# Optimization experiments

Hardware: AMD Instinct MI355X
Metric: run time of the kernel (lower is better)

Reference implementation:

```python
import jax, jax.numpy as jnp
import numpy as np


def _ln(x, w, b, eps=1e-5):
    m = x.mean(-1, keepdims=True)
    v = jnp.mean((x - m) ** 2, axis=-1, keepdims=True)
    return (x - m) * jax.lax.rsqrt(v + eps) * w + b


def _to_seq(xc, g):
    # xc: [B,Di,H,W] -> [B,L,Di]; g0: row-major fwd, g1: row-major rev,
    # g2: col-major fwd, g3: col-major rev (CrossScan_1..4)
    if g >= 2:
        xc = xc.transpose(0, 1, 3, 2)
    s = xc.reshape(xc.shape[0], xc.shape[1], -1)
    if g % 2 == 1:
        s = jnp.flip(s, -1)
    return s.transpose(0, 2, 1)


def _from_seq(y, g, H, W):
    # y: [B,L,Di] -> [B,H,W,Di], inverse of _to_seq (CrossMerge_1..4)
    if g % 2 == 1:
        y = jnp.flip(y, 1)
    Bn, L, Di = y.shape
    if g >= 2:
        return y.reshape(Bn, W, H, Di).transpose(0, 2, 1, 3)
    return y.reshape(Bn, H, W, Di)


def _sscan(dA, dBx, Cm):
    # selective scan: h_t = dA_t*h + dBx_t ; y_t = <h_t, C_t>
    # dA,dBx: [B,L,Di,S], Cm: [B,L,S] -> y: [B,L,Di]
    def step(h, inp):
        a, bx, c = inp
        h = a * h + bx
        return h, jnp.einsum('bds,bs->bd', h, c)
    h0 = jnp.zeros(dA.shape[:1] + dA.shape[2:], dA.dtype)
    _, ys = jax.lax.scan(step, h0, (dA.transpose(1, 0, 2, 3), dBx.transpose(1, 0, 2, 3), Cm.transpose(1, 0, 2)))
    return ys.transpose(1, 0, 2)


def _ss2d(xc, g, H, W, ipw, ipb, cw, cb, xpw, dtw, dtb, A_log, Ds, onw, onb, opw, opb):
    R = dtw.shape[-1]
    S = A_log.shape[-1]
    xz = xc @ ipw.T + ipb                      # [B,H,W,2*Di]
    Di = xz.shape[-1] // 2
    xi, z = xz[..., :Di], xz[..., Di:]
    xi = xi.transpose(0, 3, 1, 2)              # [B,Di,H,W]
    xi = jax.lax.conv_general_dilated(xi, cw, (1, 1), [(1, 1), (1, 1)],
                                      dimension_numbers=('NCHW', 'OIHW', 'NCHW'),
                                      feature_group_count=Di) + cb[None, :, None, None]
    xi = jax.nn.silu(xi)
    seq = _to_seq(xi, g)                       # [B,L,Di]
    xdbl = seq @ xpw.T                         # [B,L,R+2S]
    dtr, Bm, Cm = xdbl[..., :R], xdbl[..., R:R + S], xdbl[..., R + S:]
    dt = jax.nn.softplus(dtr @ dtw.T + dtb)    # [B,L,Di]
    A = -jnp.exp(A_log)                        # [Di,S]
    dA = jnp.exp(dt[..., None] * A)            # [B,L,Di,S]
    dBx = (dt * seq)[..., None] * Bm[:, :, None, :]
    y = _sscan(dA, dBx, Cm) + Ds * seq
    y = _from_seq(y, g, H, W)                  # [B,H,W,Di]
    y = _ln(y, onw, onb)
    y = y * jax.nn.silu(z)
    return y @ opw.T + opb


def setup_inputs() -> dict:
    Bn, Hh, Ww, C = 8, 96, 96, 256
    Di = C // 4
    S = 1
    R = max(1, (Di + 15) // 16)
    key = jax.random.key(0)
    ks = jax.random.split(key, 12)
    nrm = lambda k, sh, s: jax.random.normal(k, sh, jnp.float32) * s
    return {
        'x': nrm(ks[0], (Bn, Hh * Ww, C), 1.0),
        'norm_w': jnp.ones((C,), jnp.float32), 'norm_b': jnp.zeros((C,), jnp.float32),
        'fc_w': nrm(ks[1], (C, C), 0.02), 'fc_b': jnp.zeros((C,), jnp.float32),
        'conv1d_w': nrm(ks[2], (1, 1, 3), 0.3),
        'in_proj_w': nrm(ks[3], (4, 2 * Di, Di), 0.05), 'in_proj_b': jnp.zeros((4, 2 * Di), jnp.float32),
        'conv2d_w': nrm(ks[4], (4, Di, 1, 3, 3), 0.2), 'conv2d_b': jnp.zeros((4, Di), jnp.float32),
        'x_proj_w': nrm(ks[5], (4, R + 2 * S, Di), 0.05),
        'dt_w': nrm(ks[6], (4, Di, R), 0.1), 'dt_b': nrm(ks[7], (4, Di), 0.1),
        'A_log': nrm(ks[8], (4, Di, S), 0.1),
        'Ds': jnp.ones((4, Di), jnp.float32),
        'out_norm_w': jnp.ones((4, Di), jnp.float32), 'out_norm_b': jnp.zeros((4, Di), jnp.float32),
        'out_proj_w': nrm(ks[9], (4, Di, Di), 0.05), 'out_proj_b': jnp.zeros((4, Di), jnp.float32),
        'proj_w': nrm(ks[10], (C, C), 0.02), 'proj_b': jnp.zeros((C,), jnp.float32),
        'skip_scale': jnp.ones((1,), jnp.float32),
        'H': Hh, 'W': Ww,
    }


def reference(x, norm_w, norm_b, fc_w, fc_b, conv1d_w, in_proj_w, in_proj_b, conv2d_w, conv2d_b,
              x_proj_w, dt_w, dt_b, A_log, Ds, out_norm_w, out_norm_b, out_proj_w, out_proj_b,
              proj_w, proj_b, skip_scale, H, W):
    B, N, C = x.shape
    xn = _ln(x, norm_w, norm_b)
    z_avg = xn.mean(1)                         # [B,C] (permute(0,2,1).mean(2))
    yg = jax.lax.conv_general_dilated(z_avg[:, None, :], conv1d_w, (1,), [(1, 1)],
                                      dimension_numbers=('NCH', 'OIH', 'NCH'))[:, 0, :]
    gate = jax.nn.sigmoid(z_avg @ fc_w.T + fc_b + yg)   # fc_out_2 [B,C]
    xg = xn.reshape(B, H, W, C)
    Dg = C // 4
    outs = [_ss2d(xg[..., g * Dg:(g + 1) * Dg], g, H, W,
                  in_proj_w[g], in_proj_b[g], conv2d_w[g], conv2d_b[g], x_proj_w[g],
                  dt_w[g], dt_b[g], A_log[g], Ds[g], out_norm_w[g], out_norm_b[g],
                  out_proj_w[g], out_proj_b[g]) for g in range(4)]
    xm = jnp.concatenate(outs, -1) * skip_scale * xg
    xm = xm.reshape(B, N, C) * gate[:, None, :]
    xm = _ln(xm, norm_w, norm_b)
    return xm @ proj_w.T + proj_b
```

## Files before the change

### kernel.cpp

```cpp
#include <hip/hip_runtime.h>
#include <math.h>

#define HH 96
#define WWI 96
#define NN 9216
#define CC 256
#define LL 9216
#define CHK 96
#define NCH 96
#define BB 8
#define BN (BB*NN)

__device__ __forceinline__ float softplusf(float x){
    float e = expf(-fabsf(x));
    return fmaxf(x, 0.f) + log1pf(e);
}
__device__ __forceinline__ float sigmf(float x){ return 1.f / (1.f + expf(-x)); }

__device__ __forceinline__ float wredsum(float v){
    #pragma unroll
    for(int o = 32; o > 0; o >>= 1) v += __shfl_xor(v, o, 64);
    return v;
}

__device__ __forceinline__ void wredsum2(float& s, float& q){
    #pragma unroll
    for(int o = 32; o > 0; o >>= 1){
        s += __shfl_xor(s, o, 64);
        q += __shfl_xor(q, o, 64);
    }
}

__device__ __forceinline__ void chunk_walk(int g, int chunk, int& base, int& step){
    if(g == 0){ base = chunk * 96;        step = 1;   }
    else if(g == 1){ base = 9215 - chunk * 96; step = -1; }
    else if(g == 2){ base = chunk;        step = 96;  }
    else { base = 9215 - chunk;           step = -96; }
}

__global__ __launch_bounds__(256) void k_stats(const float* __restrict__ x,
                                               float* __restrict__ mrs){
    int wid = threadIdx.x >> 6, lane = threadIdx.x & 63;
    size_t row = (size_t)blockIdx.x * 4 + wid;
    float4 v = ((const float4*)(x + row * CC))[lane];
    float s = wredsum(v.x + v.y + v.z + v.w);
    float q = wredsum(v.x*v.x + v.y*v.y + v.z*v.z + v.w*v.w);
    float m = s * (1.f/256.f);
    float var = q * (1.f/256.f) - m*m;
    float rs = rsqrtf(fmaxf(var, 0.f) + 1e-5f);
    if(lane == 0){ mrs[2*row] = m; mrs[2*row+1] = rs; }
}

__global__ __launch_bounds__(256) void k_stats2(const float* __restrict__ y,
                                                float* __restrict__ mrs2){
    int wid = threadIdx.x >> 6, lane = threadIdx.x & 63;
    size_t row = (size_t)blockIdx.x * 4 + wid;
    size_t b = row / NN, n = row - b * NN;
    int g = lane >> 4, c4 = (lane & 15) * 4;
    float4 v = *(const float4*)(y + (((size_t)b*4 + g)*NN + n)*64 + c4);
    float s = wredsum(v.x + v.y + v.z + v.w);
    float q = wredsum(v.x*v.x + v.y*v.y + v.z*v.z + v.w*v.w);
    float m = s * (1.f/256.f);
    float var = q * (1.f/256.f) - m*m;
    float rs = rsqrtf(fmaxf(var, 0.f) + 1e-5f);
    if(lane == 0){ mrs2[2*row] = m; mrs2[2*row+1] = rs; }
}

__global__ __launch_bounds__(256) void k_prew(const float* __restrict__ pw,
        const float* __restrict__ nw, const float* __restrict__ nb,
        const float* __restrict__ pb, float* __restrict__ Wn,
        float* __restrict__ wsum, float* __restrict__ cvec){
    int o = threadIdx.x;
    float ws = 0.f, cc = 0.f;
    for(int k = 0; k < 256; k++){
        float w = pw[(size_t)o * 256 + k];
        float wn = w * nw[k];
        Wn[(size_t)o * 256 + k] = wn;
        ws += wn; cc += w * nb[k];
    }
    wsum[o] = ws; cvec[o] = cc + pb[o];
}

__global__ __launch_bounds__(256) void k_zavg(const float* __restrict__ x,
        const float* __restrict__ mrs, const float* __restrict__ nw,
        const float* __restrict__ nb, float* __restrict__ zpart){
    int c = threadIdx.x, b = blockIdx.y, t0 = blockIdx.x * 256;
    float nwv = nw[c], nbv = nb[c];
    float s = 0.f;
    for(int i = 0; i < 256; i++){
        size_t r = (size_t)b * NN + t0 + i;
        s += (x[r * CC + c] - mrs[2*r]) * mrs[2*r+1] * nwv + nbv;
    }
    zpart[((size_t)b * 36 + blockIdx.x) * CC + c] = s;
}

__global__ __launch_bounds__(256) void k_gate(const float* __restrict__ zpart,
        const float* __restrict__ fcw, const float* __restrict__ fcb,
        const float* __restrict__ w1d, float* __restrict__ gate){
    __shared__ float za[CC];
    int c = threadIdx.x, b = blockIdx.x;
    float s = 0.f;
    for(int t = 0; t < 36; t++) s += zpart[((size_t)b * 36 + t) * CC + c];
    za[c] = s * (1.f/(float)NN);
    __syncthreads();
    float zm1 = (c > 0)     ? za[c-1] : 0.f;
    float zp1 = (c < CC-1)  ? za[c+1] : 0.f;
    float acc = fcb[c] + w1d[0]*zm1 + w1d[1]*za[c] + w1d[2]*zp1;
    const float* wr = fcw + (size_t)c * CC;
    for(int k = 0; k < CC; k++) acc += za[k] * wr[k];
    gate[b * CC + c] = sigmf(acc);
}

__global__ __launch_bounds__(256) void k_inproj(const float* __restrict__ x,
        const float* __restrict__ mrs, const float* __restrict__ nw,
        const float* __restrict__ nb, const float* __restrict__ ipw,
        const float* __restrict__ ipb, float* __restrict__ xib,
        float* __restrict__ zbuf){
    int tile = blockIdx.x, b = blockIdx.y, g = blockIdx.z;
    int n0 = tile * 128;
    __shared__ float xs[128 * 64];
    int tid = threadIdx.x;
    for(int idx = tid; idx < 2048; idx += 256){
        int p = idx >> 4, k4 = (idx & 15) * 4;
        size_t r = (size_t)b * NN + n0 + p;
        float4 v = *(const float4*)(x + r * CC + g*64 + k4);
        float m = mrs[2*r], rs = mrs[2*r+1];
        float4 w4 = *(const float4*)(nw + g*64 + k4);
        float4 b4 = *(const float4*)(nb + g*64 + k4);
        float4 o;
        o.x = (v.x - m)*rs*w4.x + b4.x;
        o.y = (v.y - m)*rs*w4.y + b4.y;
        o.z = (v.z - m)*rs*w4.z + b4.z;
        o.w = (v.w - m)*rs*w4.w + b4.w;
        *(float4*)(xs + p*64 + k4) = o;
    }
    __syncthreads();
    int c = tid & 63, ph = tid >> 6;
    float wx[64], wz[64];
    {
        const float* wrx = ipw + ((size_t)(g*128 + c)) * 64;
        const float* wrz = ipw + ((size_t)(g*128 + 64 + c)) * 64;
        #pragma unroll
        for(int k = 0; k < 64; k++){ wx[k] = wrx[k]; wz[k] = wrz[k]; }
    }
    float bx = ipb[g*128 + c], bz = ipb[g*128 + 64 + c];
    size_t obase = ((size_t)(b*4 + g)) * NN + n0;
    for(int p = ph*32; p < ph*32 + 32; p++){
        const float4* xp = (const float4*)(xs + p*64);
        float a0 = 0.f, a1 = 0.f, z0 = 0.f, z1 = 0.f;
        #pragma unroll
        for(int k4 = 0; k4 < 16; k4 += 2){
            float4 u = xp[k4], v = xp[k4+1];
            a0 += u.x*wx[4*k4+0]; a1 += u.y*wx[4*k4+1];
            a0 += u.z*wx[4*k4+2]; a1 += u.w*wx[4*k4+3];
            z0 += u.x*wz[4*k4+0]; z1 += u.y*wz[4*k4+1];
            z0 += u.z*wz[4*k4+2]; z1 += u.w*wz[4*k4+3];
            a0 += v.x*wx[4*k4+4]; a1 += v.y*wx[4*k4+5];
            a0 += v.z*wx[4*k4+6]; a1 += v.w*wx[4*k4+7];
            z0 += v.x*wz[4*k4+4]; z1 += v.y*wz[4*k4+5];
            z0 += v.z*wz[4*k4+6]; z1 += v.w*wz[4*k4+7];
        }
        float xv = bx + a0 + a1;
        float zv = bz + z0 + z1;
        xib[(obase + p)*64 + c] = xv;
        zbuf[(obase + p)*64 + c] = zv * sigmf(zv);
    }
}

__global__ __launch_bounds__(256) void k_conv(const float* __restrict__ xib,
        const float* __restrict__ cw, const float* __restrict__ cb,
        float* __restrict__ out){
    int tile = blockIdx.x, b = blockIdx.y, g = blockIdx.z;
    int h0 = (tile/12)*8, w0 = (tile%12)*8;
    __shared__ float xs[100*64];
    int tid = threadIdx.x;
    size_t ibase = ((size_t)(b*4+g)) * NN;
    for(int i = tid; i < 6400; i += 256){
        int p = i >> 6, k = i & 63;
        int ph = h0 + p/10 - 1, pw = w0 + p%10 - 1;
        float v = 0.f;
        if(ph >= 0 && ph < HH && pw >= 0 && pw < WWI)
            v = xib[(ibase + (size_t)(ph*WWI + pw))*64 + k];
        xs[i] = v;
    }
    __syncthreads();
    int c = tid & 63, q = tid >> 6;
    float wk[9];
    const float* wp = cw + ((size_t)(g*64 + c))*9;
    #pragma unroll
    for(int j = 0; j < 9; j++) wk[j] = wp[j];
    float bias2 = cb[g*64 + c];
    for(int pi = q*16; pi < q*16+16; pi++){
        int py = pi >> 3, px = pi & 7;
        float acc = bias2;
        #pragma unroll
        for(int dy = 0; dy < 3; dy++)
            #pragma unroll
            for(int dx = 0; dx < 3; dx++)
                acc += xs[((py+dy)*10 + px+dx)*64 + c] * wk[dy*3+dx];
        float sv = acc * sigmf(acc);
        size_t r = (size_t)b*NN + (h0+py)*WWI + (w0+px);
        out[r*CC + g*64 + c] = sv;
    }
}

template<int ZPRE>
__global__ __launch_bounds__(256) void k_ipconv(const float* __restrict__ x,
        const float* __restrict__ mrs, const float* __restrict__ nw,
        const float* __restrict__ nb, const float* __restrict__ ipw,
        const float* __restrict__ ipb, const float* __restrict__ cw,
        const float* __restrict__ cb, float* __restrict__ out,
        float* __restrict__ zbuf){
    int tile = blockIdx.x, b = blockIdx.y, g = blockIdx.z;
    int h0 = (tile / 12) * 8, w0 = (tile % 12) * 8;
    __shared__ float xs[100 * 64];
    __shared__ float xi[100 * 64];
    int tid = threadIdx.x;
    for(int i = tid; i < 6400; i += 256){
        int p = i >> 6, k = i & 63;
        int ph = h0 + p / 10 - 1, pw = w0 + p % 10 - 1;
        float v = 0.f;
        if(ph >= 0 && ph < HH && pw >= 0 && pw < WWI){
            size_t r = (size_t)b * NN + ph * WWI + pw;
            v = (x[r * CC + g*64 + k] - mrs[2*r]) * mrs[2*r+1]
                * nw[g*64 + k] + nb[g*64 + k];
        }
        xs[i] = v;
    }
    __syncthreads();
    int c = tid & 63, q = tid >> 6;
    {
        float wv[64];
        const float* wr = ipw + ((size_t)(g * 128 + c)) * 64;
        #pragma unroll
        for(int k = 0; k < 64; k++) wv[k] = wr[k];
        float bias = ipb[g * 128 + c];
        for(int p = q * 25; p < q * 25 + 25; p++){
            int ph = h0 + p / 10 - 1, pw = w0 + p % 10 - 1;
            bool valid = (ph >= 0 && ph < HH && pw >= 0 && pw < WWI);
            float acc = bias;
            const float* xp = &xs[p * 64];
            #pragma unroll
            for(int k = 0; k < 64; k++) acc += xp[k] * wv[k];
            xi[p * 64 + c] = valid ? acc : 0.f;
        }
    }
    __syncthreads();
    float wk[9];
    const float* wp = cw + ((size_t)(g * 64 + c)) * 9;
    #pragma unroll
    for(int j = 0; j < 9; j++) wk[j] = wp[j];
    float bias2 = cb[g * 64 + c];
    for(int pi = q * 16; pi < q * 16 + 16; pi++){
        int py = pi >> 3, px = pi & 7;
        float acc = bias2;
        #pragma unroll
        for(int dy = 0; dy < 3; dy++)
            #pragma unroll
            for(int dx = 0; dx < 3; dx++)
                acc += xi[((py + dy) * 10 + px + dx) * 64 + c] * wk[dy*3 + dx];
        float sv = acc * sigmf(acc);
        size_t r = (size_t)b * NN + (h0 + py) * WWI + (w0 + px);
        out[r * CC + g*64 + c] = sv;
    }
    if(ZPRE){
        float wzv[64];
        const float* wr = ipw + ((size_t)(g * 128 + 64 + c)) * 64;
        #pragma unroll
        for(int k = 0; k < 64; k++) wzv[k] = wr[k];
        float zbv = ipb[g * 128 + 64 + c];
        size_t zb0 = ((size_t)(b * 4 + g)) * NN;
        for(int p16 = 0; p16 < 16; p16++){
            int p = q * 16 + p16;
            int py = p >> 3, px = p & 7;
            const float* xp = &xs[((py + 1) * 10 + (px + 1)) * 64];
            float acc = zbv;
            #pragma unroll
            for(int k = 0; k < 64; k++) acc += xp[k] * wzv[k];
            zbuf[(zb0 + (size_t)((h0 + py) * WWI + (w0 + px))) * 64 + c]
                = acc * sigmf(acc);
        }
    }
}

__global__ __launch_bounds__(64) void k_scan1(const float* __restrict__ out,
        const float* __restrict__ xpw, const float* __restrict__ dtw,
        const float* __restrict__ dtb, const float* __restrict__ alog,
        float* __restrict__ ap_out, float* __restrict__ h_out){
    int chunk = blockIdx.x, gb = blockIdx.y;
    int g = gb >> 3, b = gb & 7, d = threadIdx.x;
    __shared__ float s_seq[CHK * 65];
    __shared__ float s_xd[CHK * 6];
    __shared__ float s_w[6 * 64];
    int base, step; chunk_walk(g, chunk, base, step);
    const float* xg = out + (size_t)b * NN * CC + g * 64;
    for(int j = 0; j < CHK; j++)
        s_seq[j * 65 + d] = xg[(size_t)(base + j * step) * CC + d];
    for(int i = d; i < 384; i += 64) s_w[i] = xpw[g * 384 + i];
    __syncthreads();
    for(int idx = d; idx < CHK*6; idx += 64){
        int l = idx / 6, j = idx % 6;
        float acc = 0.f;
        const float* sr = &s_seq[l * 65];
        const float* wr = &s_w[j * 64];
        #pragma unroll
        for(int k = 0; k < 64; k++) acc += sr[k] * wr[k];
        s_xd[idx] = acc;
    }
    __syncthreads();
    int gd = g * 64 + d;
    float Av = -expf(alog[gd]);
    float db = dtb[gd];
    float w0 = dtw[gd*4], w1 = dtw[gd*4+1], w2 = dtw[gd*4+2], w3 = dtw[gd*4+3];
    float h = 0.f, apd = 1.f;
    #pragma unroll 4
    for(int l = 0; l < CHK; l++){
        const float* xd = &s_xd[l * 6];
        float xv = s_seq[l*65 + d];
        float dt = softplusf(xd[0]*w0 + xd[1]*w1 + xd[2]*w2 + xd[3]*w3 + db);
        float a = expf(dt * Av);
        h = a*h + dt*xv*xd[4];
        apd *= a;
    }
    int ob = (gb * NCH + chunk) * 64 + d;
    ap_out[ob] = apd; h_out[ob] = h;
}

__global__ __launch_bounds__(256) void k_scan2(const float* __restrict__ ap,
        const float* __restrict__ he, float* __restrict__ hinit){
    int idx = blockIdx.x * 256 + threadIdx.x;
    int gb = idx >> 6, d = idx & 63;
    float h = 0.f;
    for(int c = 0; c < NCH; c++){
        int o = (gb * NCH + c) * 64 + d;
        hinit[o] = h;
        h = ap[o]*h + he[o];
    }
}

template<int ZPRE>
__global__ __launch_bounds__(64) void k_scan3(float* __restrict__ out,
        const float* __restrict__ x, const float* __restrict__ mrs,
        const float* __restrict__ nw, const float* __restrict__ nb,
        const float* __restrict__ ipw, const float* __restrict__ ipb,
        const float* __restrict__ xpw, const float* __restrict__ dtw,
        const float* __restrict__ dtb, const float* __restrict__ alog,
        const float* __restrict__ Dsp, const float* __restrict__ onw,
        const float* __restrict__ onb, const float* __restrict__ hinit,
        const float* __restrict__ zbuf){
    int chunk = blockIdx.x, gb = blockIdx.y;
    int g = gb >> 3, b = gb & 7, d = threadIdx.x;
    __shared__ float s_seq[CHK * 65];
    __shared__ float s_xd[CHK * 6];
    __shared__ float s_w[6 * 64];
    __shared__ float xnt[(ZPRE ? 1 : CHK) * 65];
    int base, step; chunk_walk(g, chunk, base, step);
    float* xg = out + (size_t)b * NN * CC + g * 64;
    for(int j = 0; j < CHK; j++)
        s_seq[j * 65 + d] = xg[(size_t)(base + j * step) * CC + d];
    if(!ZPRE){
        float nwv = nw[g*64 + d], nbv = nb[g*64 + d];
        for(int j = 0; j < CHK; j++){
            int n = base + j * step;
            size_t r = (size_t)b * NN + n;
            xnt[j * 65 + d] = (x[r * CC + g*64 + d] - mrs[2*r]) * mrs[2*r+1] * nwv + nbv;
        }
    }
    for(int i = d; i < 384; i += 64) s_w[i] = xpw[g * 384 + i];
    __syncthreads();
    for(int idx = d; idx < CHK*6; idx += 64){
        int l = idx / 6, j = idx % 6;
        float acc = 0.f;
        const float* sr = &s_seq[l * 65];
        const float* wr = &s_w[j * 64];
        #pragma unroll
        for(int k = 0; k < 64; k++) acc += sr[k] * wr[k];
        s_xd[idx] = acc;
    }
    __syncthreads();
    int gd = g * 64 + d;
    float Av = -expf(alog[gd]);
    float db = dtb[gd];
    float Dv = Dsp[gd];
    float w0 = dtw[gd*4], w1 = dtw[gd*4+1], w2 = dtw[gd*4+2], w3 = dtw[gd*4+3];
    float h = hinit[(gb * NCH + chunk) * 64 + d];
    #pragma unroll 4
    for(int l = 0; l < CHK; l++){
        const float* xd = &s_xd[l * 6];
        float xv = s_seq[l*65 + d];
        float dt = softplusf(xd[0]*w0 + xd[1]*w1 + xd[2]*w2 + xd[3]*w3 + db);
        float a = expf(dt * Av);
        h = a*h + dt*xv*xd[4];
        s_seq[l*65 + d] = h * xd[5] + Dv * xv;
    }
    float wON = onw[gd], bON = onb[gd];
    float wz[ZPRE ? 1 : 64];
    float zb = 0.f;
    if(!ZPRE){
        const float* wr = ipw + ((size_t)(g * 128 + 64 + d)) * 64;
        #pragma unroll
        for(int k = 0; k < 64; k++) wz[k] = wr[k];
        zb = ipb[g * 128 + 64 + d];
    }
    const float* zp = zbuf + (((size_t)(b * 4 + g)) * NN) * 64 + d;
    #pragma unroll 4
    for(int l = 0; l < CHK; l++){
        float y = s_seq[l*65 + d];
        float s = y, q = y * y;
        wredsum2(s, q);
        float m = s * (1.f/64.f);
        float var = q * (1.f/64.f) - m*m;
        float rs = rsqrtf(fmaxf(var, 0.f) + 1e-5f);
        float lny = (y - m) * rs * wON + bON;
        int n = base + l * step;
        float zs;
        if(ZPRE){
            zs = zp[(size_t)n * 64];
        } else {
            float z = zb;
            const float* xp = &xnt[l * 65];
            #pragma unroll
            for(int k = 0; k < 64; k++) z += xp[k] * wz[k];
            zs = z * sigmf(z);
        }
        xg[(size_t)n * CC + d] = lny * zs;
    }
}

template<int TOZ>
__global__ __launch_bounds__(64) void k_out2(float* __restrict__ out,
        const float* __restrict__ x, const float* __restrict__ mrs,
        const float* __restrict__ nw, const float* __restrict__ nb,
        const float* __restrict__ opw, const float* __restrict__ opb,
        const float* __restrict__ gate, const float* __restrict__ skip,
        float* __restrict__ zo){
    int tile = blockIdx.x, b = blockIdx.y, g = blockIdx.z;
    int n0 = tile * 64, t = threadIdx.x;
    __shared__ float ly[64 * 65];
    __shared__ float xnt[64 * 65];
    float* xg = out + (size_t)b * NN * CC + g * 64;
    float nwv = nw[g*64 + t], nbv = nb[g*64 + t];
    for(int p = 0; p < 64; p++){
        size_t r = (size_t)b * NN + n0 + p;
        ly[p * 65 + t] = xg[(size_t)(n0 + p) * CC + t];
        xnt[p * 65 + t] = (x[r * CC + g*64 + t] - mrs[2*r]) * mrs[2*r+1] * nwv + nbv;
    }
    __syncthreads();
    float wv[64];
    const float* wr = opw + ((size_t)(g * 64 + t)) * 64;
    #pragma unroll
    for(int k = 0; k < 64; k++) wv[k] = wr[k];
    float bias = opb[g * 64 + t];
    float gv = gate[b * CC + g*64 + t];
    float sk = skip[0];
    for(int p = 0; p < 64; p++){
        float acc = bias;
        const float* yp = &ly[p * 65];
        #pragma unroll
        for(int k = 0; k < 64; k++) acc += yp[k] * wv[k];
        float res = acc * sk * xnt[p * 65 + t] * gv;
        if(TOZ)
            zo[((size_t)(b*4 + g)*NN + n0 + p)*64 + t] = res;
        else
            xg[(size_t)(n0 + p) * CC + t] = res;
    }
}

__global__ __launch_bounds__(256) void k_final(float* __restrict__ out,
        const float* __restrict__ nw, const float* __restrict__ nb,
        const float* __restrict__ pw, const float* __restrict__ pb){
    __shared__ float A[16 * 256];
    __shared__ float ps[256], pq[256];
    __shared__ float mrow[16], rrow[16];
    int n0 = blockIdx.x * 16;
    for(int i = threadIdx.x; i < 4096; i += 256)
        A[i] = out[(size_t)n0 * CC + i];
    __syncthreads();
    {
        int r = threadIdx.x >> 4, t16 = threadIdx.x & 15;
        float s = 0.f, q = 0.f;
        for(int j = 0; j < 16; j++){
            float v = A[r*256 + t16*16 + j];
            s += v; q += v*v;
        }
        ps[threadIdx.x] = s; pq[threadIdx.x] = q;
    }
    __syncthreads();
    if(threadIdx.x < 16){
        float ss = 0.f, qq = 0.f;
        for(int j = 0; j < 16; j++){ ss += ps[threadIdx.x*16 + j]; qq += pq[threadIdx.x*16 + j]; }
        float m = ss * (1.f/256.f);
        float var = qq * (1.f/256.f) - m*m;
        mrow[threadIdx.x] = m;
        rrow[threadIdx.x] = rsqrtf(fmaxf(var, 0.f) + 1e-5f);
    }
    __syncthreads();
    for(int i = threadIdx.x; i < 4096; i += 256){
        int r = i >> 8, c = i & 255;
        A[i] = (A[i] - mrow[r]) * rrow[r] * nw[c] + nb[c];
    }
    __syncthreads();
    int o = threadIdx.x;
    float acc[16];
    #pragma unroll
    for(int p = 0; p < 16; p++) acc[p] = 0.f;
    for(int kt = 0; kt < 4; kt++){
        float wv[64];
        const float4* wr = (const float4*)(pw + (size_t)o * CC + kt * 64);
        #pragma unroll
        for(int j = 0; j < 16; j++){
            float4 tq = wr[j];
            wv[4*j+0] = tq.x; wv[4*j+1] = tq.y;
            wv[4*j+2] = tq.z; wv[4*j+3] = tq.w;
        }
        #pragma unroll
        for(int p = 0; p < 16; p++){
            const float* ar = &A[p*256 + kt*64];
            float a = 0.f;
            #pragma unroll
            for(int k = 0; k < 64; k++) a += ar[k] * wv[k];
            acc[p] += a;
        }
    }
    float pbv = pb[o];
    #pragma unroll
    for(int p = 0; p < 16; p++)
        out[(size_t)(n0 + p) * CC + o] = acc[p] + pbv;
}

__global__ __launch_bounds__(256) void k_final2(const float* __restrict__ y,
        const float* __restrict__ mrs2, const float* __restrict__ Wn,
        const float* __restrict__ wsum, const float* __restrict__ cvec,
        float* __restrict__ out){
    int o = threadIdx.x;
    int r0 = blockIdx.x * 16;
    int b  = r0 / NN;
    int n0 = r0 - b * NN;
    float acc[16];
    #pragma unroll
    for(int r = 0; r < 16; r++) acc[r] = 0.f;
    for(int kt = 0; kt < 4; kt++){
        float wv[64];
        const float4* wr = (const float4*)(Wn + (size_t)o * 256 + kt * 64);
        #pragma unroll
        for(int j = 0; j < 16; j++){
            float4 t4 = wr[j];
            wv[4*j+0] = t4.x; wv[4*j+1] = t4.y;
            wv[4*j+2] = t4.z; wv[4*j+3] = t4.w;
        }
        const float* ab = y + ((size_t)(b*4 + kt)*NN + n0) * 64;
        #pragma unroll 4
        for(int r = 0; r < 16; r++){
            const float* ar = ab + (size_t)r * 64;
            float s0 = 0.f, s1 = 0.f;
            #pragma unroll
            for(int j = 0; j < 32; j++){
                s0 += ar[j]      * wv[j];
                s1 += ar[j + 32] * wv[j + 32];
            }
            acc[r] += s0 + s1;
        }
    }
    float wso = wsum[o], co = cvec[o];
    #pragma unroll
    for(int r = 0; r < 16; r++){
        float m  = mrs2[2*(size_t)(r0 + r)];
        float rs = mrs2[2*(size_t)(r0 + r) + 1];
        out[(size_t)(r0 + r) * CC + o] = rs * acc[r] - m * rs * wso + co;
    }
}

extern "C" void kernel_launch(void* const* d_in, const int* in_sizes, int n_in,
                              void* d_out, int out_size, void* d_ws, size_t ws_size,
                              hipStream_t stream){
    const float* x    = (const float*)d_in[0];
    const float* nw   = (const float*)d_in[1];
    const float* nb   = (const float*)d_in[2];
    const float* fcw  = (const float*)d_in[3];
    const float* fcb  = (const float*)d_in[4];
    const float* w1d  = (const float*)d_in[5];
    const float* ipw  = (const float*)d_in[6];
    const float* ipb  = (const float*)d_in[7];
    const float* cw   = (const float*)d_in[8];
    const float* cb   = (const float*)d_in[9];
    const float* xpw  = (const float*)d_in[10];
    const float* dtw  = (const float*)d_in[11];
    const float* dtb  = (const float*)d_in[12];
    const float* alog = (const float*)d_in[13];
    const float* Dsp  = (const float*)d_in[14];
    const float* onw  = (const float*)d_in[15];
    const float* onb  = (const float*)d_in[16];
    const float* opw  = (const float*)d_in[17];
    const float* opb  = (const float*)d_in[18];
    const float* pw   = (const float*)d_in[19];
    const float* pb   = (const float*)d_in[20];
    const float* skip = (const float*)d_in[21];

    char* base = (char*)d_ws;
    float* mrs  = (float*)base;
    float* gate = (float*)(base +  589824ull);
    float* ap   = (float*)(base +  598016ull);
    float* he   = (float*)(base + 1384448ull);
    float* hi   = (float*)(base + 2170880ull);
    float* zbuf = (float*)(base + 2957312ull);
    float* mrs2 = (float*)(base + 78454784ull);
    float* Wn   = (float*)(base + 79044608ull);
    float* wsum = (float*)(base + 79306752ull);
    float* cvec = (float*)(base + 79307776ull);
    float* xib  = (float*)(base + 79308800ull);
    float* zpart = ap;
    float* out  = (float*)d_out;
    (void)in_sizes; (void)n_in; (void)out_size;

    const size_t T1 = 78454784ull;
    const size_t T2 = 79308800ull;
    const size_t T3 = 154806272ull;
    bool usez    = ws_size >= T1;
    bool usef2   = ws_size >= T2;
    bool usesplit= ws_size >= T3;

    if(usef2)
        k_prew<<<1, 256, 0, stream>>>(pw, nw, nb, pb, Wn, wsum, cvec);
    k_stats <<<18432, 256, 0, stream>>>(x, mrs);
    k_zavg  <<<dim3(36, 8), 256, 0, stream>>>(x, mrs, nw, nb, zpart);
    k_gate  <<<8, 256, 0, stream>>>(zpart, fcw, fcb, w1d, gate);
    if(usesplit){
        k_inproj<<<dim3(72, 8, 4), 256, 0, stream>>>(x, mrs, nw, nb, ipw, ipb,
                                                     xib, zbuf);
        k_conv  <<<dim3(144, 8, 4), 256, 0, stream>>>(xib, cw, cb, out);
    } else if(usez){
        k_ipconv<1><<<dim3(144, 8, 4), 256, 0, stream>>>(x, mrs, nw, nb, ipw, ipb,
                                                         cw, cb, out, zbuf);
    } else {
        k_ipconv<0><<<dim3(144, 8, 4), 256, 0, stream>>>(x, mrs, nw, nb, ipw, ipb,
                                                         cw, cb, out, zbuf);
    }
    k_scan1 <<<dim3(96, 32), 64, 0, stream>>>(out, xpw, dtw, dtb, alog, ap, he);
    k_scan2 <<<8, 256, 0, stream>>>(ap, he, hi);
    if(usez){
        k_scan3<1><<<dim3(96, 32), 64, 0, stream>>>(out, x, mrs, nw, nb, ipw, ipb,
                                                    xpw, dtw, dtb, alog, Dsp, onw,
                                                    onb, hi, zbuf);
    } else {
        k_scan3<0><<<dim3(96, 32), 64, 0, stream>>>(out, x, mrs, nw, nb, ipw, ipb,
                                                    xpw, dtw, dtb, alog, Dsp, onw,
                                                    onb, hi, zbuf);
    }
    if(usef2){
        k_out2<1><<<dim3(144, 8, 4), 64, 0, stream>>>(out, x, mrs, nw, nb, opw, opb,
                                                      gate, skip, zbuf);
        k_stats2<<<18432, 256, 0, stream>>>(zbuf, mrs2);
        k_final2<<<4608, 256, 0, stream>>>(zbuf, mrs2, Wn, wsum, cvec, out);
    } else {
        k_out2<0><<<dim3(144, 8, 4), 64, 0, stream>>>(out, x, mrs, nw, nb, opw, opb,
                                                      gate, skip, zbuf);
        k_final <<<4608, 256, 0, stream>>>(out, nw, nb, pw, pb);
    }
}
```

Before: 1.332 ms.

## Fuse out-projection with final LayerNorm statistics into a new 256-thread kernel

Result: faster. 1.226 ms (median of 2 runs) (-7.9%).

```diff
diff --git a/kernel.cpp b/kernel.cpp
--- a/kernel.cpp
+++ b/kernel.cpp
@@ -49,21 +49,6 @@
     float var = q * (1.f/256.f) - m*m;
     float rs = rsqrtf(fmaxf(var, 0.f) + 1e-5f);
     if(lane == 0){ mrs[2*row] = m; mrs[2*row+1] = rs; }
-}
-
-__global__ __launch_bounds__(256) void k_stats2(const float* __restrict__ y,
-                                                float* __restrict__ mrs2){
-    int wid = threadIdx.x >> 6, lane = threadIdx.x & 63;
-    size_t row = (size_t)blockIdx.x * 4 + wid;
-    size_t b = row / NN, n = row - b * NN;
-    int g = lane >> 4, c4 = (lane & 15) * 4;
-    float4 v = *(const float4*)(y + (((size_t)b*4 + g)*NN + n)*64 + c4);
-    float s = wredsum(v.x + v.y + v.z + v.w);
-    float q = wredsum(v.x*v.x + v.y*v.y + v.z*v.z + v.w*v.w);
-    float m = s * (1.f/256.f);
-    float var = q * (1.f/256.f) - m*m;
-    float rs = rsqrtf(fmaxf(var, 0.f) + 1e-5f);
-    if(lane == 0){ mrs2[2*row] = m; mrs2[2*row+1] = rs; }
 }
 
 __global__ __launch_bounds__(256) void k_prew(const float* __restrict__ pw,
@@ -427,13 +412,11 @@
     }
 }
 
-template<int TOZ>
 __global__ __launch_bounds__(64) void k_out2(float* __restrict__ out,
         const float* __restrict__ x, const float* __restrict__ mrs,
         const float* __restrict__ nw, const float* __restrict__ nb,
         const float* __restrict__ opw, const float* __restrict__ opb,
-        const float* __restrict__ gate, const float* __restrict__ skip,
-        float* __restrict__ zo){
+        const float* __restrict__ gate, const float* __restrict__ skip){
     int tile = blockIdx.x, b = blockIdx.y, g = blockIdx.z;
     int n0 = tile * 64, t = threadIdx.x;
     __shared__ float ly[64 * 65];
@@ -458,11 +441,74 @@
         const float* yp = &ly[p * 65];
         #pragma unroll
         for(int k = 0; k < 64; k++) acc += yp[k] * wv[k];
-        float res = acc * sk * xnt[p * 65 + t] * gv;
-        if(TOZ)
-            zo[((size_t)(b*4 + g)*NN + n0 + p)*64 + t] = res;
-        else
-            xg[(size_t)(n0 + p) * CC + t] = res;
+        xg[(size_t)(n0 + p) * CC + t] = acc * sk * xnt[p * 65 + t] * gv;
+    }
+}
+
+__global__ __launch_bounds__(256) void k_out3(const float* __restrict__ yin,
+        const float* __restrict__ x, const float* __restrict__ mrs,
+        const float* __restrict__ nw, const float* __restrict__ nb,
+        const float* __restrict__ opw, const float* __restrict__ opb,
+        const float* __restrict__ gate, const float* __restrict__ skip,
+        float* __restrict__ zo, float* __restrict__ mrs2){
+    __shared__ float ps[16 * 4], pq[16 * 4];
+    int o = threadIdx.x;
+    int g = o >> 6, c = o & 63;
+    int r0 = blockIdx.x * 16;
+    int b  = r0 / NN;
+    int n0 = r0 - b * NN;
+    float wv[64];
+    {
+        const float4* wr = (const float4*)(opw + ((size_t)(g*64 + c)) * 64);
+        #pragma unroll
+        for(int j = 0; j < 16; j++){
+            float4 t4 = wr[j];
+            wv[4*j+0] = t4.x; wv[4*j+1] = t4.y;
+            wv[4*j+2] = t4.z; wv[4*j+3] = t4.w;
+        }
+    }
+    float acc[16];
+    const float* ab = yin + ((size_t)b * NN + n0) * CC + g * 64;
+    #pragma unroll 4
+    for(int r = 0; r < 16; r++){
+        const float4* ar = (const float4*)(ab + (size_t)r * CC);
+        float s0 = 0.f, s1 = 0.f;
+        #pragma unroll
+        for(int j = 0; j < 8; j++){
+            float4 u = ar[j], v = ar[j + 8];
+            s0 += u.x*wv[4*j+0]  + u.y*wv[4*j+1]  + u.z*wv[4*j+2]  + u.w*wv[4*j+3];
+            s1 += v.x*wv[32+4*j] + v.y*wv[33+4*j] + v.z*wv[34+4*j] + v.w*wv[35+4*j];
+        }
+        acc[r] = s0 + s1;
+    }
+    float bias = opb[g*64 + c];
+    float gv = gate[b * CC + g*64 + c];
+    float sk = skip[0];
+    float nwv = nw[g*64 + c], nbv = nb[g*64 + c];
+    size_t zbase = ((size_t)(b*4 + g)) * NN + n0;
+    #pragma unroll
+    for(int r = 0; r < 16; r++){
+        size_t row = (size_t)r0 + r;
+        float xv = x[row * CC + g*64 + c];
+        float xn = (xv - mrs[2*row]) * mrs[2*row+1] * nwv + nbv;
+        float res = (acc[r] + bias) * sk * xn * gv;
+        acc[r] = res;
+        zo[(zbase + r) * 64 + c] = res;
+    }
+    #pragma unroll
+    for(int r = 0; r < 16; r++){
+        float s = acc[r], q = acc[r] * acc[r];
+        wredsum2(s, q);
+        if(c == 0){ ps[r*4 + g] = s; pq[r*4 + g] = q; }
+    }
+    __syncthreads();
+    if(o < 16){
+        float ss = ps[o*4] + ps[o*4+1] + ps[o*4+2] + ps[o*4+3];
+        float qq = pq[o*4] + pq[o*4+1] + pq[o*4+2] + pq[o*4+3];
+        float m = ss * (1.f/256.f);
+        float var = qq * (1.f/256.f) - m*m;
+        mrs2[2*((size_t)r0 + o)]     = m;
+        mrs2[2*((size_t)r0 + o) + 1] = rsqrtf(fmaxf(var, 0.f) + 1e-5f);
     }
 }
 
@@ -647,13 +693,12 @@
                                                     onb, hi, zbuf);
     }
     if(usef2){
-        k_out2<1><<<dim3(144, 8, 4), 64, 0, stream>>>(out, x, mrs, nw, nb, opw, opb,
-                                                      gate, skip, zbuf);
-        k_stats2<<<18432, 256, 0, stream>>>(zbuf, mrs2);
+        k_out3  <<<4608, 256, 0, stream>>>(out, x, mrs, nw, nb, opw, opb,
+                                           gate, skip, zbuf, mrs2);
         k_final2<<<4608, 256, 0, stream>>>(zbuf, mrs2, Wn, wsum, cvec, out);
     } else {
-        k_out2<0><<<dim3(144, 8, 4), 64, 0, stream>>>(out, x, mrs, nw, nb, opw, opb,
-                                                      gate, skip, zbuf);
+        k_out2  <<<dim3(144, 8, 4), 64, 0, stream>>>(out, x, mrs, nw, nb, opw, opb,
+                                                     gate, skip);
         k_final <<<4608, 256, 0, stream>>>(out, nw, nb, pw, pb);
     }
 }
```
